# Kernel optimization log

Measured on AMD Instinct MI355X. Metric: run time of the kernel, lower is better.

Reference implementation:

```python
import jax, jax.numpy as jnp
import numpy as np

B, S, D, H = 2, 2048, 2048, 16
HD = D // H  # 128


def _rope_tables(seq_len, head_dim, base=10000.0):
    inv_freq = 1.0 / (base ** (np.arange(0, head_dim, 2, dtype=np.float32) / head_dim))
    t = np.arange(seq_len, dtype=np.float32)
    freqs = np.outer(t, inv_freq)  # [S, HD/2]
    return jnp.asarray(np.cos(freqs)), jnp.asarray(np.sin(freqs))


def setup_inputs() -> dict:
    key = jax.random.key(0)
    ks = jax.random.split(key, 5)
    std = 0.02
    inp = {
        "x": jax.random.normal(ks[0], (B, S, D), jnp.float32),
        "wq": jax.random.normal(ks[1], (D, D), jnp.float32) * std,
        "bq": jnp.zeros((D,), jnp.float32),
        "wk": jax.random.normal(ks[2], (D, D), jnp.float32) * std,
        "bk": jnp.zeros((D,), jnp.float32),
        "wv": jax.random.normal(ks[3], (D, D), jnp.float32) * std,
        "bv": jnp.zeros((D,), jnp.float32),
        "wo": jax.random.normal(ks[4], (D, D), jnp.float32) * std,
        "bo": jnp.zeros((D,), jnp.float32),
    }
    cos, sin = _rope_tables(S, HD)
    inp["freqs_cos"], inp["freqs_sin"] = cos, sin
    return inp


def _apply_rope(t, cos, sin):
    # t: [B,S,H,HD]; cos/sin: [S,HD/2] -> broadcast [1,S,1,HD/2]
    tp = t.reshape(*t.shape[:-1], HD // 2, 2)
    t1, t2 = tp[..., 0], tp[..., 1]
    c = cos[None, :, None, :]
    s = sin[None, :, None, :]
    out = jnp.stack([t1 * c - t2 * s, t1 * s + t2 * c], axis=-1)
    return out.reshape(t.shape)


def reference(x, wq, bq, wk, bk, wv, bv, wo, bo, freqs_cos, freqs_sin):
    b, s, d = x.shape
    q = (x @ wq.T + bq).reshape(b, s, H, HD)
    k = (x @ wk.T + bk).reshape(b, s, H, HD)
    v = (x @ wv.T + bv).reshape(b, s, H, HD)
    q = _apply_rope(q, freqs_cos, freqs_sin)
    k = _apply_rope(k, freqs_cos, freqs_sin)
    # causal SDPA: scores [B,H,S,S]
    scale = 1.0 / jnp.sqrt(jnp.asarray(HD, x.dtype))
    scores = jnp.einsum("bqhd,bkhd->bhqk", q, k) * scale
    causal = jnp.tril(jnp.ones((s, s), bool))
    scores = jnp.where(causal[None, None], scores, jnp.asarray(-1e30, scores.dtype))
    attn = jax.nn.softmax(scores.astype(jnp.float32), axis=-1).astype(x.dtype)
    out = jnp.einsum("bhqk,bkhd->bqhd", attn, v).reshape(b, s, d)
    return out @ wo.T + bo
```

## Files before the change

kernel.cpp:

```cpp
#include <hip/hip_runtime.h>


typedef __attribute__((ext_vector_type(8))) short short8;
typedef __attribute__((ext_vector_type(4))) float f32x4;
typedef __attribute__((ext_vector_type(16))) float f32x16;
typedef __attribute__((ext_vector_type(4))) unsigned short u16x4;
typedef __attribute__((ext_vector_type(8))) unsigned short u16x8;

constexpr int Bc = 2, Sc = 2048, Dc = 2048, Hc = 16, HDc = 128;
constexpr int Mc = Bc * Sc;
constexpr int Nc = Dc, Kc = Dc;
constexpr float QSCL = 0.08838834764831845f * 1.4426950408889634f;

__device__ __forceinline__ unsigned short f2bf(float f) {
    union { float f; unsigned u; } x; x.f = f;
    unsigned r = x.u + 0x7FFFu + ((x.u >> 16) & 1u);
    return (unsigned short)(r >> 16);
}

__device__ __forceinline__ void g2lds16(const void* g, void* l) {
    __builtin_amdgcn_global_load_lds(
        (const __attribute__((address_space(1))) void*)g,
        (__attribute__((address_space(3))) void*)l, 16, 0, 0);
}

__device__ __forceinline__ void cvt_body(const float* __restrict__ in,
                                         unsigned short* __restrict__ out, int i) {
    f32x4 a = *((const f32x4*)in + (size_t)i * 2);
    f32x4 b = *((const f32x4*)in + (size_t)i * 2 + 1);
    u16x8 o;
    o[0] = f2bf(a[0]); o[1] = f2bf(a[1]); o[2] = f2bf(a[2]); o[3] = f2bf(a[3]);
    o[4] = f2bf(b[0]); o[5] = f2bf(b[1]); o[6] = f2bf(b[2]); o[7] = f2bf(b[3]);
    *((u16x8*)out + i) = o;
}

__global__ __launch_bounds__(256) void cvt_f32_bf16(
    const float* __restrict__ in, unsigned short* __restrict__ out, int n8) {
    int i = blockIdx.x * 256 + threadIdx.x;
    if (i >= n8) return;
    cvt_body(in, out, i);
}

__global__ __launch_bounds__(256) void cvt_batch(
    const float* __restrict__ x,  unsigned short* __restrict__ xo,
    const float* __restrict__ w0, unsigned short* __restrict__ o0,
    const float* __restrict__ w1, unsigned short* __restrict__ o1,
    const float* __restrict__ w2, unsigned short* __restrict__ o2,
    const float* __restrict__ w3, unsigned short* __restrict__ o3) {
    const int which = blockIdx.y;
    const float* in; unsigned short* out; int n8;
    if (which == 0)      { in = x;  out = xo; n8 = (Mc * Dc) / 8; }
    else if (which == 1) { in = w0; out = o0; n8 = (Dc * Dc) / 8; }
    else if (which == 2) { in = w1; out = o1; n8 = (Dc * Dc) / 8; }
    else if (which == 3) { in = w2; out = o2; n8 = (Dc * Dc) / 8; }
    else                 { in = w3; out = o3; n8 = (Dc * Dc) / 8; }
    int i = blockIdx.x * 256 + threadIdx.x;
    if (i >= n8) return;
    cvt_body(in, out, i);
}

template <int MODE>
__global__ __launch_bounds__(256) void gemm_nt(
    const unsigned short* __restrict__ A, const unsigned short* __restrict__ W,
    const float* __restrict__ bias, const float* __restrict__ rc,
    const float* __restrict__ rs, void* __restrict__ outp) {
    __shared__ __align__(16) unsigned short As[128 * 64];
    __shared__ __align__(16) unsigned short Bs[128 * 64];
    const int tid = threadIdx.x;
    const int w = tid >> 6, l = tid & 63;
    const int wm = w >> 1, wn = w & 1;
    const int lrow = l & 15, lhi = l >> 4;
    const int m0 = blockIdx.y * 128, n0 = blockIdx.x * 128;

    f32x4 acc[4][4];
#pragma unroll
    for (int i = 0; i < 4; ++i)
#pragma unroll
        for (int j = 0; j < 4; ++j) acc[i][j] = (f32x4){0.f, 0.f, 0.f, 0.f};

    for (int k0 = 0; k0 < Kc; k0 += 64) {
        __syncthreads();
#pragma unroll
        for (int i = 0; i < 4; ++i) {
            int s = i * 256 + tid;
            int row = s >> 3, c = s & 7;
            int cg = (c ^ (row & 7)) * 8;
            g2lds16(A + (size_t)(m0 + row) * Kc + k0 + cg,
                    &As[(size_t)(i * 256 + (w << 6)) * 8]);
            g2lds16(W + (size_t)(n0 + row) * Kc + k0 + cg,
                    &Bs[(size_t)(i * 256 + (w << 6)) * 8]);
        }
        __syncthreads();
#pragma unroll
        for (int kk = 0; kk < 2; ++kk) {
            short8 af[4], bf[4];
#pragma unroll
            for (int i = 0; i < 4; ++i) {
                int ra = wm * 64 + i * 16 + lrow;
                af[i] = *(const short8*)&As[ra * 64 + (((kk * 4 + lhi) ^ (ra & 7)) << 3)];
                int rb = wn * 64 + i * 16 + lrow;
                bf[i] = *(const short8*)&Bs[rb * 64 + (((kk * 4 + lhi) ^ (rb & 7)) << 3)];
            }
#pragma unroll
            for (int i = 0; i < 4; ++i)
#pragma unroll
                for (int j = 0; j < 4; ++j)
                    acc[i][j] = __builtin_amdgcn_mfma_f32_16x16x32_bf16(
                        af[i], bf[j], acc[i][j], 0, 0, 0);
        }
    }

#pragma unroll
    for (int i = 0; i < 4; ++i) {
#pragma unroll
        for (int j = 0; j < 4; ++j) {
            int gm0 = m0 + wm * 64 + i * 16 + lhi * 4;
            int gn  = n0 + wn * 64 + j * 16 + lrow;
            float bv = bias[gn];
            if (MODE == 0 || MODE == 1) {
                unsigned short* o = (unsigned short*)outp;
                int fi = (gn & (HDc - 1)) >> 1;
#pragma unroll
                for (int r = 0; r < 4; ++r) {
                    int gm = gm0 + r;
                    float v = acc[i][j][r] + bv;
                    float p = __shfl_xor(v, 1);
                    int pos = gm & (Sc - 1);
                    float cz = rc[pos * (HDc / 2) + fi];
                    float sz = rs[pos * (HDc / 2) + fi];
                    float ov = (gn & 1) ? (p * sz + v * cz) : (v * cz - p * sz);
                    if (MODE == 0) ov *= QSCL;
                    o[(size_t)gm * Nc + gn] = f2bf(ov);
                }
            } else if (MODE == 2) {
                unsigned short* o = (unsigned short*)outp;
                int b = gm0 >> 11, sb = gm0 & (Sc - 1);
                u16x4 pk;
#pragma unroll
                for (int r = 0; r < 4; ++r) pk[r] = f2bf(acc[i][j][r] + bv);
                *(u16x4*)&o[((size_t)b * Dc + gn) * Sc + sb] = pk;
            } else {
                float* o = (float*)outp;
#pragma unroll
                for (int r = 0; r < 4; ++r)
                    o[(size_t)(gm0 + r) * Nc + gn] = acc[i][j][r] + bv;
            }
        }
    }
}

__global__ __launch_bounds__(256, 2) void attn_fwd5(
    const unsigned short* __restrict__ Q, const unsigned short* __restrict__ Kb,
    const unsigned short* __restrict__ Vt, unsigned short* __restrict__ O) {
    __shared__ __align__(16) unsigned short Ks[2][64 * 128];
    __shared__ __align__(16) unsigned short Vs[2][128 * 64];
    const int tid = threadIdx.x;
    const int w = tid >> 6, l = tid & 63;
    const int ql = l & 31, Hh = l >> 5;
    const int bh = blockIdx.x;
    const int y = blockIdx.y;
    const int qt = (y < 8) ? y : (23 - y);
    const int b = bh >> 4, h = bh & 15;

    const unsigned short* Kbase = Kb + ((size_t)b * Sc) * Dc + h * HDc;
    const unsigned short* Vbase = Vt + ((size_t)b * Dc + h * HDc) * Sc;

#define STAGE(tt, kd, vd) {                                                    \
    const unsigned short* Kt = Kbase + (size_t)(tt) * 64 * Dc;                 \
    const unsigned short* Vp = Vbase + (tt) * 64;                              \
    _Pragma("unroll")                                                          \
    for (int i_ = 0; i_ < 4; ++i_) {                                           \
        int p_ = i_ * 256 + tid;                                               \
        int rK = p_ >> 4, sK = p_ & 15;                                        \
        g2lds16(Kt + (size_t)rK * Dc + ((sK ^ (rK & 15)) << 3),                \
                (kd) + (i_ * 256 + (w << 6)) * 8);                             \
        int rV = p_ >> 3, sV = p_ & 7;                                         \
        g2lds16(Vp + (size_t)rV * Sc + ((sV ^ (rV & 7)) << 3),                 \
                (vd) + (i_ * 256 + (w << 6)) * 8);                             \
    } }

#define PVSTEP(PC, HB, KS) {                                                   \
    int X0, X1, Y0, Y1;                                                        \
    asm("v_cvt_pk_bf16_f32 %0, %1, %2" : "=v"(X0) : "v"(PC[HB+0]), "v"(PC[HB+1])); \
    asm("v_cvt_pk_bf16_f32 %0, %1, %2" : "=v"(X1) : "v"(PC[HB+2]), "v"(PC[HB+3])); \
    asm("v_cvt_pk_bf16_f32 %0, %1, %2" : "=v"(Y0) : "v"(PC[HB+4]), "v"(PC[HB+5])); \
    asm("v_cvt_pk_bf16_f32 %0, %1, %2" : "=v"(Y1) : "v"(PC[HB+6]), "v"(PC[HB+7])); \
    asm("v_permlane32_swap_b32 %0, %1" : "+v"(X0), "+v"(Y0));                  \
    asm("v_permlane32_swap_b32 %0, %1" : "+v"(X1), "+v"(Y1));                  \
    union { int i[4]; short8 s; } pf_;                                         \
    pf_.i[0] = X0; pf_.i[1] = X1; pf_.i[2] = Y0; pf_.i[3] = Y1;                \
    _Pragma("unroll")                                                          \
    for (int dc_ = 0; dc_ < 4; ++dc_) {                                        \
        int rr = 32 * dc_ + ql;                                                \
        short8 vf = *(const short8*)&Vbuf[rr * 64 + (((2*(KS)+Hh) ^ (rr & 7)) << 3)]; \
        accv[dc_] = __builtin_amdgcn_mfma_f32_32x32x16_bf16(vf, pf_.s, accv[dc_], 0, 0, 0); \
    } }

    const int qw0 = qt * 128 + w * 32;
    const int qg = qw0 + ql;

    short8 qf[8];
    {
        const unsigned short* qp = Q + ((size_t)(b * Sc + qg)) * Dc + h * HDc;
#pragma unroll
        for (int dc = 0; dc < 8; ++dc)
            qf[dc] = *(const short8*)(qp + dc * 16 + Hh * 8);
    }
    f32x16 accv[4];
#pragma unroll
    for (int i = 0; i < 4; ++i) accv[i] = (f32x16)(0.f);
    float mrun = -3.0e38f, lrun = 0.f;
    const int nt = 2 * qt + 2;

    STAGE(0, Ks[0], Vs[0]);
    for (int t = 0; t < nt; ++t) {
        if (t + 1 < nt) {
            STAGE(t + 1, Ks[(t + 1) & 1], Vs[(t + 1) & 1]);
            asm volatile("s_waitcnt vmcnt(8)" ::: "memory");
        } else {
            asm volatile("s_waitcnt vmcnt(0)" ::: "memory");
        }
        __builtin_amdgcn_s_barrier();

        const unsigned short* Kbuf = Ks[t & 1];
        const unsigned short* Vbuf = Vs[t & 1];
        const int kb0 = t * 64;
        if (kb0 <= qw0 + 31) {
            f32x16 a0 = (f32x16)(0.f), a1 = (f32x16)(0.f);
            __builtin_amdgcn_s_setprio(1);
#pragma unroll
            for (int dc = 0; dc < 8; ++dc) {
                int r0 = ql, r1 = 32 + ql, sl = dc * 2 + Hh;
                short8 k0 = *(const short8*)&Kbuf[r0 * 128 + ((sl ^ (r0 & 15)) << 3)];
                short8 k1 = *(const short8*)&Kbuf[r1 * 128 + ((sl ^ (r1 & 15)) << 3)];
                a0 = __builtin_amdgcn_mfma_f32_32x32x16_bf16(k0, qf[dc], a0, 0, 0, 0);
                a1 = __builtin_amdgcn_mfma_f32_32x32x16_bf16(k1, qf[dc], a1, 0, 0, 0);
            }
            __builtin_amdgcn_s_setprio(0);
            if (t >= 2 * qt) {
#pragma unroll
                for (int r = 0; r < 16; ++r) {
                    int kl = (r & 3) + 8 * (r >> 2) + 4 * Hh;
                    if (kb0 + kl > qg)      a0[r] = -3.0e38f;
                    if (kb0 + 32 + kl > qg) a1[r] = -3.0e38f;
                }
            }
            float m8[8];
#pragma unroll
            for (int r = 0; r < 8; ++r)
                m8[r] = fmaxf(fmaxf(a0[r], a0[r + 8]), fmaxf(a1[r], a1[r + 8]));
            float m4a = fmaxf(m8[0], m8[1]), m4b = fmaxf(m8[2], m8[3]);
            float m4c = fmaxf(m8[4], m8[5]), m4d = fmaxf(m8[6], m8[7]);
            float pm = fmaxf(fmaxf(m4a, m4b), fmaxf(m4c, m4d));
            pm = fmaxf(pm, __shfl_xor(pm, 32));
            if (!__all(pm - mrun <= 8.0f)) {
                float mnew = fmaxf(mrun, pm);
                float fs = exp2f(mrun - mnew);
                mrun = mnew;
                lrun *= fs;
#pragma unroll
                for (int dc = 0; dc < 4; ++dc)
#pragma unroll
                    for (int r = 0; r < 16; ++r) accv[dc][r] *= fs;
            }
            float p0[16], p1[16];
#pragma unroll
            for (int r = 0; r < 16; ++r) p0[r] = exp2f(a0[r] - mrun);
#pragma unroll
            for (int r = 0; r < 16; ++r) p1[r] = exp2f(a1[r] - mrun);
            float s8[8];
#pragma unroll
            for (int r = 0; r < 8; ++r)
                s8[r] = (p0[r] + p0[r + 8]) + (p1[r] + p1[r + 8]);
            float s4a = s8[0] + s8[1], s4b = s8[2] + s8[3];
            float s4c = s8[4] + s8[5], s4d = s8[6] + s8[7];
            float ps = (s4a + s4b) + (s4c + s4d);
            lrun += ps + __shfl_xor(ps, 32);
            __builtin_amdgcn_s_setprio(1);
            PVSTEP(p0, 0, 0); PVSTEP(p0, 8, 1);
            PVSTEP(p1, 0, 2); PVSTEP(p1, 8, 3);
            __builtin_amdgcn_s_setprio(0);
        }
        __builtin_amdgcn_s_barrier();
    }
    float inv = 1.f / lrun;
    unsigned short* Op = O + ((size_t)(b * Sc + qg)) * Dc + h * HDc;
#pragma unroll
    for (int dc = 0; dc < 4; ++dc)
#pragma unroll
        for (int rg = 0; rg < 4; ++rg) {
            int d0 = 32 * dc + 8 * rg + 4 * Hh;
            u16x4 pk;
#pragma unroll
            for (int j = 0; j < 4; ++j) pk[j] = f2bf(accv[dc][rg * 4 + j] * inv);
            *(u16x4*)(Op + d0) = pk;
        }
#undef STAGE
#undef PVSTEP
}

extern "C" void kernel_launch(void* const* d_in, const int* in_sizes, int n_in,
                              void* d_out, int out_size, void* d_ws, size_t ws_size,
                              hipStream_t stream) {
    const float* x  = (const float*)d_in[0];
    const float* wq = (const float*)d_in[1];
    const float* bq = (const float*)d_in[2];
    const float* wk = (const float*)d_in[3];
    const float* bk = (const float*)d_in[4];
    const float* wv = (const float*)d_in[5];
    const float* bv = (const float*)d_in[6];
    const float* wo = (const float*)d_in[7];
    const float* bo = (const float*)d_in[8];
    const float* rc = (const float*)d_in[9];
    const float* rs = (const float*)d_in[10];

    const size_t NE = (size_t)Mc * Dc;
    const size_t NW = (size_t)Dc * Dc;

    unsigned short* xb = (unsigned short*)d_ws;
    unsigned short* qb = xb + NE;
    unsigned short* kb = qb + NE;
    unsigned short* vt = kb + NE;
    unsigned short* wb = vt + NE;

    const int ne8 = (int)(NE / 8), nw8 = (int)(NW / 8);
    dim3 gg(Nc / 128, Mc / 128), tb(256);
    const bool big_ws = ws_size >= (4 * NE + 4 * NW) * sizeof(unsigned short);

    if (big_ws) {
        unsigned short* wqb = wb;
        unsigned short* wkb = wb + NW;
        unsigned short* wvb = wb + 2 * NW;
        unsigned short* wob = wb + 3 * NW;
        cvt_batch<<<dim3(ne8 / 256, 5), tb, 0, stream>>>(
            x, xb, wq, wqb, wk, wkb, wv, wvb, wo, wob);
        gemm_nt<0><<<gg, tb, 0, stream>>>(xb, wqb, bq, rc, rs, qb);
        gemm_nt<1><<<gg, tb, 0, stream>>>(xb, wkb, bk, rc, rs, kb);
        gemm_nt<2><<<gg, tb, 0, stream>>>(xb, wvb, bv, rc, rs, vt);
        attn_fwd5<<<dim3(Bc * Hc, 16), tb, 0, stream>>>(qb, kb, vt, xb);
        gemm_nt<3><<<gg, tb, 0, stream>>>(xb, wob, bo, rc, rs, d_out);
    } else {
        cvt_f32_bf16<<<dim3(ne8 / 256), tb, 0, stream>>>(x, xb, ne8);
        cvt_f32_bf16<<<dim3(nw8 / 256), tb, 0, stream>>>(wq, wb, nw8);
        gemm_nt<0><<<gg, tb, 0, stream>>>(xb, wb, bq, rc, rs, qb);
        cvt_f32_bf16<<<dim3(nw8 / 256), tb, 0, stream>>>(wk, wb, nw8);
        gemm_nt<1><<<gg, tb, 0, stream>>>(xb, wb, bk, rc, rs, kb);
        cvt_f32_bf16<<<dim3(nw8 / 256), tb, 0, stream>>>(wv, wb, nw8);
        gemm_nt<2><<<gg, tb, 0, stream>>>(xb, wb, bv, rc, rs, vt);
        attn_fwd5<<<dim3(Bc * Hc, 16), tb, 0, stream>>>(qb, kb, vt, xb);
        cvt_f32_bf16<<<dim3(nw8 / 256), tb, 0, stream>>>(wo, wb, nw8);
        gemm_nt<3><<<gg, tb, 0, stream>>>(xb, wb, bo, rc, rs, d_out);
    }
}
```

Measured before the change: 272.1 us.

## Split long causal attention tiles across two blocks with LSE combine kernel

Result: no change. 274.1 us (+0.7%).

```diff
diff --git a/kernel.cpp b/kernel.cpp
--- a/kernel.cpp
+++ b/kernel.cpp
@@ -4,6 +4,7 @@
 typedef __attribute__((ext_vector_type(8))) short short8;
 typedef __attribute__((ext_vector_type(4))) float f32x4;
 typedef __attribute__((ext_vector_type(16))) float f32x16;
+typedef __attribute__((ext_vector_type(2))) unsigned short u16x2;
 typedef __attribute__((ext_vector_type(4))) unsigned short u16x4;
 typedef __attribute__((ext_vector_type(8))) unsigned short u16x8;
 
@@ -16,6 +17,9 @@
     union { float f; unsigned u; } x; x.f = f;
     unsigned r = x.u + 0x7FFFu + ((x.u >> 16) & 1u);
     return (unsigned short)(r >> 16);
+}
+__device__ __forceinline__ float bf2f(unsigned short u) {
+    union { float f; unsigned u; } x; x.u = (unsigned)u << 16; return x.f;
 }
 
 __device__ __forceinline__ void g2lds16(const void* g, void* l) {
@@ -149,23 +153,7 @@
     }
 }
 
-__global__ __launch_bounds__(256, 2) void attn_fwd5(
-    const unsigned short* __restrict__ Q, const unsigned short* __restrict__ Kb,
-    const unsigned short* __restrict__ Vt, unsigned short* __restrict__ O) {
-    __shared__ __align__(16) unsigned short Ks[2][64 * 128];
-    __shared__ __align__(16) unsigned short Vs[2][128 * 64];
-    const int tid = threadIdx.x;
-    const int w = tid >> 6, l = tid & 63;
-    const int ql = l & 31, Hh = l >> 5;
-    const int bh = blockIdx.x;
-    const int y = blockIdx.y;
-    const int qt = (y < 8) ? y : (23 - y);
-    const int b = bh >> 4, h = bh & 15;
-
-    const unsigned short* Kbase = Kb + ((size_t)b * Sc) * Dc + h * HDc;
-    const unsigned short* Vbase = Vt + ((size_t)b * Dc + h * HDc) * Sc;
-
-#define STAGE(tt, kd, vd) {                                                    \
+#define ATTN_STAGE(tt, kd, vd) {                                               \
     const unsigned short* Kt = Kbase + (size_t)(tt) * 64 * Dc;                 \
     const unsigned short* Vp = Vbase + (tt) * 64;                              \
     _Pragma("unroll")                                                          \
@@ -179,7 +167,7 @@
                 (vd) + (i_ * 256 + (w << 6)) * 8);                             \
     } }
 
-#define PVSTEP(PC, HB, KS) {                                                   \
+#define ATTN_PVSTEP(PC, HB, KS) {                                              \
     int X0, X1, Y0, Y1;                                                        \
     asm("v_cvt_pk_bf16_f32 %0, %1, %2" : "=v"(X0) : "v"(PC[HB+0]), "v"(PC[HB+1])); \
     asm("v_cvt_pk_bf16_f32 %0, %1, %2" : "=v"(X1) : "v"(PC[HB+2]), "v"(PC[HB+3])); \
@@ -196,6 +184,86 @@
         accv[dc_] = __builtin_amdgcn_mfma_f32_32x32x16_bf16(vf, pf_.s, accv[dc_], 0, 0, 0); \
     } }
 
+#define ATTN_TILE_BODY(Kbuf, Vbuf, kb0)                                        \
+    {                                                                          \
+        f32x16 a0 = (f32x16)(0.f), a1 = (f32x16)(0.f);                         \
+        __builtin_amdgcn_s_setprio(1);                                         \
+        _Pragma("unroll")                                                      \
+        for (int dc = 0; dc < 8; ++dc) {                                       \
+            int r0 = ql, r1 = 32 + ql, sl = dc * 2 + Hh;                       \
+            short8 k0 = *(const short8*)&Kbuf[r0 * 128 + ((sl ^ (r0 & 15)) << 3)]; \
+            short8 k1 = *(const short8*)&Kbuf[r1 * 128 + ((sl ^ (r1 & 15)) << 3)]; \
+            a0 = __builtin_amdgcn_mfma_f32_32x32x16_bf16(k0, qf[dc], a0, 0, 0, 0); \
+            a1 = __builtin_amdgcn_mfma_f32_32x32x16_bf16(k1, qf[dc], a1, 0, 0, 0); \
+        }                                                                      \
+        __builtin_amdgcn_s_setprio(0);                                         \
+        if ((kb0) >= 2 * qt * 64) {                                            \
+            _Pragma("unroll")                                                  \
+            for (int r = 0; r < 16; ++r) {                                     \
+                int kl = (r & 3) + 8 * (r >> 2) + 4 * Hh;                      \
+                if ((kb0) + kl > qg)      a0[r] = -3.0e38f;                    \
+                if ((kb0) + 32 + kl > qg) a1[r] = -3.0e38f;                    \
+            }                                                                  \
+        }                                                                      \
+        float m8[8];                                                           \
+        _Pragma("unroll")                                                      \
+        for (int r = 0; r < 8; ++r)                                            \
+            m8[r] = fmaxf(fmaxf(a0[r], a0[r + 8]), fmaxf(a1[r], a1[r + 8]));   \
+        float m4a = fmaxf(m8[0], m8[1]), m4b = fmaxf(m8[2], m8[3]);            \
+        float m4c = fmaxf(m8[4], m8[5]), m4d = fmaxf(m8[6], m8[7]);            \
+        float pm = fmaxf(fmaxf(m4a, m4b), fmaxf(m4c, m4d));                    \
+        pm = fmaxf(pm, __shfl_xor(pm, 32));                                    \
+        if (!__all(pm - mrun <= 8.0f)) {                                       \
+            float mnew = fmaxf(mrun, pm);                                      \
+            float fs = exp2f(mrun - mnew);                                     \
+            mrun = mnew;                                                       \
+            lrun *= fs;                                                        \
+            _Pragma("unroll")                                                  \
+            for (int dc = 0; dc < 4; ++dc)                                     \
+                _Pragma("unroll")                                              \
+                for (int r = 0; r < 16; ++r) accv[dc][r] *= fs;                \
+        }                                                                      \
+        float p0[16], p1[16];                                                  \
+        _Pragma("unroll")                                                      \
+        for (int r = 0; r < 16; ++r) p0[r] = exp2f(a0[r] - mrun);              \
+        _Pragma("unroll")                                                      \
+        for (int r = 0; r < 16; ++r) p1[r] = exp2f(a1[r] - mrun);              \
+        float s8[8];                                                           \
+        _Pragma("unroll")                                                      \
+        for (int r = 0; r < 8; ++r)                                            \
+            s8[r] = (p0[r] + p0[r + 8]) + (p1[r] + p1[r + 8]);                 \
+        float s4a = s8[0] + s8[1], s4b = s8[2] + s8[3];                        \
+        float s4c = s8[4] + s8[5], s4d = s8[6] + s8[7];                        \
+        float ps = (s4a + s4b) + (s4c + s4d);                                  \
+        lrun += ps + __shfl_xor(ps, 32);                                       \
+        __builtin_amdgcn_s_setprio(1);                                         \
+        ATTN_PVSTEP(p0, 0, 0); ATTN_PVSTEP(p0, 8, 1);                          \
+        ATTN_PVSTEP(p1, 0, 2); ATTN_PVSTEP(p1, 8, 3);                          \
+        __builtin_amdgcn_s_setprio(0);                                         \
+    }
+
+__global__ __launch_bounds__(256, 2) void attn_part(
+    const unsigned short* __restrict__ Q, const unsigned short* __restrict__ Kb,
+    const unsigned short* __restrict__ Vt, unsigned short* __restrict__ O,
+    unsigned short* __restrict__ pacc, float* __restrict__ pml) {
+    __shared__ __align__(16) unsigned short Ks[2][64 * 128];
+    __shared__ __align__(16) unsigned short Vs[2][128 * 64];
+    const int tid = threadIdx.x;
+    const int w = tid >> 6, l = tid & 63;
+    const int ql = l & 31, Hh = l >> 5;
+    const int bh = blockIdx.x;
+    const int slot = blockIdx.y;
+    int qt, part, np;
+    if (slot < 16) { qt = 15 - (slot >> 1); part = slot & 1; np = 2; }
+    else           { qt = 23 - slot;        part = 0;        np = 1; }
+    const int nt   = 2 * qt + 2;
+    const int tbeg = part ? (qt + 1) : 0;
+    const int tend = (np == 2 && part == 0) ? (qt + 1) : nt;
+    const int b = bh >> 4, h = bh & 15;
+
+    const unsigned short* Kbase = Kb + ((size_t)b * Sc) * Dc + h * HDc;
+    const unsigned short* Vbase = Vt + ((size_t)b * Dc + h * HDc) * Sc;
+
     const int qw0 = qt * 128 + w * 32;
     const int qg = qw0 + ql;
 
@@ -210,77 +278,129 @@
 #pragma unroll
     for (int i = 0; i < 4; ++i) accv[i] = (f32x16)(0.f);
     float mrun = -3.0e38f, lrun = 0.f;
-    const int nt = 2 * qt + 2;
-
-    STAGE(0, Ks[0], Vs[0]);
-    for (int t = 0; t < nt; ++t) {
-        if (t + 1 < nt) {
-            STAGE(t + 1, Ks[(t + 1) & 1], Vs[(t + 1) & 1]);
+
+    ATTN_STAGE(tbeg, Ks[0], Vs[0]);
+    for (int t = tbeg; t < tend; ++t) {
+        const int cur = (t - tbeg) & 1;
+        if (t + 1 < tend) {
+            ATTN_STAGE(t + 1, Ks[cur ^ 1], Vs[cur ^ 1]);
             asm volatile("s_waitcnt vmcnt(8)" ::: "memory");
         } else {
             asm volatile("s_waitcnt vmcnt(0)" ::: "memory");
         }
         __builtin_amdgcn_s_barrier();
 
+        const unsigned short* Kbuf = Ks[cur];
+        const unsigned short* Vbuf = Vs[cur];
+        const int kb0 = t * 64;
+        if (kb0 <= qw0 + 31) ATTN_TILE_BODY(Kbuf, Vbuf, kb0);
+        __builtin_amdgcn_s_barrier();
+    }
+
+    if (np == 1) {
+        float inv = 1.f / lrun;
+        unsigned short* Op = O + ((size_t)(b * Sc + qg)) * Dc + h * HDc;
+#pragma unroll
+        for (int dc = 0; dc < 4; ++dc)
+#pragma unroll
+            for (int rg = 0; rg < 4; ++rg) {
+                int d0 = 32 * dc + 8 * rg + 4 * Hh;
+                u16x4 pk;
+#pragma unroll
+                for (int j = 0; j < 4; ++j) pk[j] = f2bf(accv[dc][rg * 4 + j] * inv);
+                *(u16x4*)(Op + d0) = pk;
+            }
+    } else {
+        const int jslot = ((bh << 3) + (qt - 8)) * 2 + part;
+        unsigned short* pa = pacc + (size_t)jslot * (128 * 128) + (w * 32 + ql) * 128;
+#pragma unroll
+        for (int dc = 0; dc < 4; ++dc)
+#pragma unroll
+            for (int rg = 0; rg < 4; ++rg) {
+                u16x4 pk;
+#pragma unroll
+                for (int j = 0; j < 4; ++j) pk[j] = f2bf(accv[dc][rg * 4 + j]);
+                *(u16x4*)&pa[32 * dc + 8 * rg + 4 * Hh] = pk;
+            }
+        if (Hh == 0) {
+            float* pm2 = pml + (size_t)jslot * 256 + (w * 32 + ql) * 2;
+            pm2[0] = mrun; pm2[1] = lrun;
+        }
+    }
+}
+
+__global__ __launch_bounds__(256) void attn_combine(
+    const unsigned short* __restrict__ pacc, const float* __restrict__ pml,
+    unsigned short* __restrict__ O) {
+    const int w = threadIdx.x >> 6, l = threadIdx.x & 63;
+    const int idx = blockIdx.x * 4 + w;
+    const int jp = idx >> 7, row = idx & 127;
+    const int bh = jp >> 3, qt = (jp & 7) + 8;
+    const int b = bh >> 4, h = bh & 15;
+    const unsigned short* a0 = pacc + ((size_t)jp * 2) * (128 * 128) + row * 128;
+    const unsigned short* a1 = a0 + 128 * 128;
+    const float* ml0 = pml + ((size_t)jp * 2) * 256 + row * 2;
+    const float* ml1 = ml0 + 256;
+    float m0 = ml0[0], l0 = ml0[1], m1 = ml1[0], l1 = ml1[1];
+    float M = fmaxf(m0, m1);
+    float w0 = exp2f(m0 - M), w1 = exp2f(m1 - M);
+    float inv = 1.f / (l0 * w0 + l1 * w1);
+    int d = l * 2;
+    u16x2 v0 = *(const u16x2*)&a0[d];
+    u16x2 v1 = *(const u16x2*)&a1[d];
+    u16x2 pk;
+    pk[0] = f2bf((bf2f(v0[0]) * w0 + bf2f(v1[0]) * w1) * inv);
+    pk[1] = f2bf((bf2f(v0[1]) * w0 + bf2f(v1[1]) * w1) * inv);
+    int qrow = qt * 128 + row;
+    *(u16x2*)(O + ((size_t)(b * Sc + qrow)) * Dc + h * HDc + d) = pk;
+}
+
+__global__ __launch_bounds__(256, 2) void attn_fwd5(
+    const unsigned short* __restrict__ Q, const unsigned short* __restrict__ Kb,
+    const unsigned short* __restrict__ Vt, unsigned short* __restrict__ O) {
+    __shared__ __align__(16) unsigned short Ks[2][64 * 128];
+    __shared__ __align__(16) unsigned short Vs[2][128 * 64];
+    const int tid = threadIdx.x;
+    const int w = tid >> 6, l = tid & 63;
+    const int ql = l & 31, Hh = l >> 5;
+    const int bh = blockIdx.x;
+    const int y = blockIdx.y;
+    const int qt = (y < 8) ? y : (23 - y);
+    const int b = bh >> 4, h = bh & 15;
+
+    const unsigned short* Kbase = Kb + ((size_t)b * Sc) * Dc + h * HDc;
+    const unsigned short* Vbase = Vt + ((size_t)b * Dc + h * HDc) * Sc;
+
+    const int qw0 = qt * 128 + w * 32;
+    const int qg = qw0 + ql;
+
+    short8 qf[8];
+    {
+        const unsigned short* qp = Q + ((size_t)(b * Sc + qg)) * Dc + h * HDc;
+#pragma unroll
+        for (int dc = 0; dc < 8; ++dc)
+            qf[dc] = *(const short8*)(qp + dc * 16 + Hh * 8);
+    }
+    f32x16 accv[4];
+#pragma unroll
+    for (int i = 0; i < 4; ++i) accv[i] = (f32x16)(0.f);
+    float mrun = -3.0e38f, lrun = 0.f;
+    const int nt = 2 * qt + 2;
+
+    ATTN_STAGE(0, Ks[0], Vs[0]);
+    for (int t = 0; t < nt; ++t) {
+        if (t + 1 < nt) {
+            ATTN_STAGE(t + 1, Ks[(t + 1) & 1], Vs[(t + 1) & 1]);
+            asm volatile("s_waitcnt vmcnt(8)" ::: "memory");
+        } else {
+            asm volatile("s_waitcnt vmcnt(0)" ::: "memory");
+        }
+        __builtin_amdgcn_s_barrier();
+
         const unsigned short* Kbuf = Ks[t & 1];
         const unsigned short* Vbuf = Vs[t & 1];
         const int kb0 = t * 64;
-        if (kb0 <= qw0 + 31) {
-            f32x16 a0 = (f32x16)(0.f), a1 = (f32x16)(0.f);
-            __builtin_amdgcn_s_setprio(1);
-#pragma unroll
-            for (int dc = 0; dc < 8; ++dc) {
-                int r0 = ql, r1 = 32 + ql, sl = dc * 2 + Hh;
-                short8 k0 = *(const short8*)&Kbuf[r0 * 128 + ((sl ^ (r0 & 15)) << 3)];
-                short8 k1 = *(const short8*)&Kbuf[r1 * 128 + ((sl ^ (r1 & 15)) << 3)];
-                a0 = __builtin_amdgcn_mfma_f32_32x32x16_bf16(k0, qf[dc], a0, 0, 0, 0);
-                a1 = __builtin_amdgcn_mfma_f32_32x32x16_bf16(k1, qf[dc], a1, 0, 0, 0);
-            }
-            __builtin_amdgcn_s_setprio(0);
-            if (t >= 2 * qt) {
-#pragma unroll
-                for (int r = 0; r < 16; ++r) {
-                    int kl = (r & 3) + 8 * (r >> 2) + 4 * Hh;
-                    if (kb0 + kl > qg)      a0[r] = -3.0e38f;
-                    if (kb0 + 32 + kl > qg) a1[r] = -3.0e38f;
-                }
-            }
-            float m8[8];
-#pragma unroll
-            for (int r = 0; r < 8; ++r)
-                m8[r] = fmaxf(fmaxf(a0[r], a0[r + 8]), fmaxf(a1[r], a1[r + 8]));
-            float m4a = fmaxf(m8[0], m8[1]), m4b = fmaxf(m8[2], m8[3]);
-            float m4c = fmaxf(m8[4], m8[5]), m4d = fmaxf(m8[6], m8[7]);
-            float pm = fmaxf(fmaxf(m4a, m4b), fmaxf(m4c, m4d));
-            pm = fmaxf(pm, __shfl_xor(pm, 32));
-            if (!__all(pm - mrun <= 8.0f)) {
-                float mnew = fmaxf(mrun, pm);
-                float fs = exp2f(mrun - mnew);
-                mrun = mnew;
-                lrun *= fs;
-#pragma unroll
-                for (int dc = 0; dc < 4; ++dc)
-#pragma unroll
-                    for (int r = 0; r < 16; ++r) accv[dc][r] *= fs;
-            }
-            float p0[16], p1[16];
-#pragma unroll
-            for (int r = 0; r < 16; ++r) p0[r] = exp2f(a0[r] - mrun);
-#pragma unroll
-            for (int r = 0; r < 16; ++r) p1[r] = exp2f(a1[r] - mrun);
-            float s8[8];
-#pragma unroll
-            for (int r = 0; r < 8; ++r)
-                s8[r] = (p0[r] + p0[r + 8]) + (p1[r] + p1[r + 8]);
-            float s4a = s8[0] + s8[1], s4b = s8[2] + s8[3];
-            float s4c = s8[4] + s8[5], s4d = s8[6] + s8[7];
-            float ps = (s4a + s4b) + (s4c + s4d);
-            lrun += ps + __shfl_xor(ps, 32);
-            __builtin_amdgcn_s_setprio(1);
-            PVSTEP(p0, 0, 0); PVSTEP(p0, 8, 1);
-            PVSTEP(p1, 0, 2); PVSTEP(p1, 8, 3);
-            __builtin_amdgcn_s_setprio(0);
-        }
+        if (kb0 <= qw0 + 31) ATTN_TILE_BODY(Kbuf, Vbuf, kb0);
         __builtin_amdgcn_s_barrier();
     }
     float inv = 1.f / lrun;
@@ -295,8 +415,6 @@
             for (int j = 0; j < 4; ++j) pk[j] = f2bf(accv[dc][rg * 4 + j] * inv);
             *(u16x4*)(Op + d0) = pk;
         }
-#undef STAGE
-#undef PVSTEP
 }
 
 extern "C" void kernel_launch(void* const* d_in, const int* in_sizes, int n_in,
@@ -332,12 +450,15 @@
         unsigned short* wkb = wb + NW;
         unsigned short* wvb = wb + 2 * NW;
         unsigned short* wob = wb + 3 * NW;
+        unsigned short* pacc = wb;
+        float* pml = (float*)(wb + 2 * NW);
         cvt_batch<<<dim3(ne8 / 256, 5), tb, 0, stream>>>(
             x, xb, wq, wqb, wk, wkb, wv, wvb, wo, wob);
         gemm_nt<0><<<gg, tb, 0, stream>>>(xb, wqb, bq, rc, rs, qb);
         gemm_nt<1><<<gg, tb, 0, stream>>>(xb, wkb, bk, rc, rs, kb);
         gemm_nt<2><<<gg, tb, 0, stream>>>(xb, wvb, bv, rc, rs, vt);
-        attn_fwd5<<<dim3(Bc * Hc, 16), tb, 0, stream>>>(qb, kb, vt, xb);
+        attn_part<<<dim3(Bc * Hc, 24), tb, 0, stream>>>(qb, kb, vt, xb, pacc, pml);
+        attn_combine<<<dim3(32 * 8 * 128 / 4), tb, 0, stream>>>(pacc, pml, xb);
         gemm_nt<3><<<gg, tb, 0, stream>>>(xb, wob, bo, rc, rs, d_out);
     } else {
         cvt_f32_bf16<<<dim3(ne8 / 256), tb, 0, stream>>>(x, xb, ne8);
```
